# Kernel tuning notes

Hardware: AMD Instinct MI355X
Metric: run time of the kernel (lower is better)

Reference implementation:

```python
import jax, jax.numpy as jnp
import numpy as np


def setup_inputs() -> dict:
    key = jax.random.key(0)
    kx, ks = jax.random.split(key)
    M, N, D = 8192, 8192, 512
    X = jax.random.normal(kx, (M, D), dtype=jnp.float32)
    svs = jax.random.normal(ks, (N, D), dtype=jnp.float32)
    # scale = 1/(2*sigma^2); a plausible fitted value for standard-normal data
    scale = jnp.asarray(0.01, dtype=jnp.float32)
    return {"X": X, "svs": svs, "scale": scale}


def reference(X, svs, scale):
    N, D = svs.shape
    x2 = jnp.sum(X * X, axis=-1, keepdims=True)          # [M, 1]
    s2 = jnp.sum(svs * svs, axis=-1)                      # [N]
    dist2 = x2 + s2[None, :] - 2.0 * (X @ svs.T)          # [M, N]
    dist2 = jnp.maximum(dist2, 0.0)
    log_p = (jax.scipy.special.logsumexp(-scale * dist2, axis=-1)
             - jnp.log(jnp.asarray(N, dtype=X.dtype))
             + (D / 2) * jnp.log(scale / jnp.pi))
    return log_p
```

## Files before the change

### kernel.cpp

```cpp
#include <hip/hip_runtime.h>
#include <hip/hip_bf16.h>
#include <hip/hip_fp8.h>
#include <math.h>

typedef __attribute__((ext_vector_type(4))) int   int4v;
typedef __attribute__((ext_vector_type(8))) int   int8v;
typedef __attribute__((ext_vector_type(4))) float f32x4;

#define BM 128
#define BN 128
#define BK 128

__global__ __launch_bounds__(256) void prep_kernel(
    const float* __restrict__ X, const float* __restrict__ S,
    unsigned char* __restrict__ Xq, unsigned char* __restrict__ Sq,
    float* __restrict__ x2, float* __restrict__ s2,
    float* __restrict__ rowsum, int M, int R, int Dv)
{
    const int gid  = blockIdx.x * 256 + threadIdx.x;
    const int nthr = gridDim.x * 256;

    for (int i = gid; i < M; i += nthr) rowsum[i] = 0.f;

    const int lane = threadIdx.x & 63;
    const int wid  = gid >> 6;
    const int nw   = nthr >> 6;

    for (int row = wid; row < R; row += nw) {
        const float* rp;
        unsigned char* op;
        float* sq;
        if (row < M) { rp = X + (size_t)row * Dv;       op = Xq + (size_t)row * Dv;       sq = x2 + row; }
        else         { rp = S + (size_t)(row - M) * Dv; op = Sq + (size_t)(row - M) * Dv; sq = s2 + (row - M); }

        float acc = 0.f;
        for (int k = lane * 8; k < Dv; k += 64 * 8) {
            float4 v0 = *(const float4*)(rp + k);
            float4 v1 = *(const float4*)(rp + k + 4);
            acc += v0.x * v0.x + v0.y * v0.y + v0.z * v0.z + v0.w * v0.w;
            acc += v1.x * v1.x + v1.y * v1.y + v1.z * v1.z + v1.w * v1.w;
            union { __hip_fp8_e4m3 h[8]; uint2 u; } pk;
            pk.h[0] = __hip_fp8_e4m3(v0.x);
            pk.h[1] = __hip_fp8_e4m3(v0.y);
            pk.h[2] = __hip_fp8_e4m3(v0.z);
            pk.h[3] = __hip_fp8_e4m3(v0.w);
            pk.h[4] = __hip_fp8_e4m3(v1.x);
            pk.h[5] = __hip_fp8_e4m3(v1.y);
            pk.h[6] = __hip_fp8_e4m3(v1.z);
            pk.h[7] = __hip_fp8_e4m3(v1.w);
            *(uint2*)(op + k) = pk.u;
        }
#pragma unroll
        for (int off = 1; off < 64; off <<= 1)
            acc += __shfl_xor(acc, off, 64);
        if (lane == 0) *sq = acc;
    }
}

template<int DVC>
__global__ __launch_bounds__(256, 3) void kde_gemm_kernel(
    const unsigned char* __restrict__ Xq,
    const unsigned char* __restrict__ Sq,
    const float* __restrict__ x2,
    const float* __restrict__ s2,
    const float* __restrict__ scale_p,
    float* __restrict__ rowsum,
    int M, int N, int Dv)
{
    const int D = DVC ? DVC : Dv;

    __shared__ char smem[32768];
    unsigned char* As = (unsigned char*)smem;
    unsigned char* Bs = (unsigned char*)(smem + 16384);

    const int tid  = threadIdx.x;
    const int wave = tid >> 6;
    const int lane = tid & 63;
    const int quad = lane >> 4;
    const int l16  = lane & 15;

    const int m0 = blockIdx.x * BM;
    const int n0 = blockIdx.y * BN;
    const int wm = (wave & 1) * 64;
    const int wn = (wave >> 1) * 64;

    const float sc = *scale_p;

    f32x4 acc[4][4] = {};

    const int srow0 = wave * 8 + (lane >> 3);
    const int cg    = (lane & 7) ^ (lane >> 3);
    const unsigned char* gA = Xq + (size_t)(m0 + srow0) * D + cg * 16;
    const unsigned char* gB = Sq + (size_t)(n0 + srow0) * D + cg * 16;

#pragma unroll
    for (int k0 = 0; k0 < D; k0 += BK) {
        __syncthreads();
#pragma unroll
        for (int rd = 0; rd < 4; ++rd)
            __builtin_amdgcn_global_load_lds(
                (const __attribute__((address_space(1))) void*)(gA + (size_t)rd * 32 * D + k0),
                (__attribute__((address_space(3))) void*)(smem + rd * 4096 + wave * 1024),
                16, 0, 0);
#pragma unroll
        for (int rd = 0; rd < 4; ++rd)
            __builtin_amdgcn_global_load_lds(
                (const __attribute__((address_space(1))) void*)(gB + (size_t)rd * 32 * D + k0),
                (__attribute__((address_space(3))) void*)(smem + 16384 + rd * 4096 + wave * 1024),
                16, 0, 0);
        __syncthreads();

        const int e = l16 & 7;
        int8v a_frag[4], b_frag[4];
#pragma unroll
        for (int mi = 0; mi < 4; ++mi) {
            const unsigned char* rowp = As + (wm + mi * 16 + l16) * 128;
            int4v lo = *(const int4v*)(rowp + ((2 * quad)     ^ e) * 16);
            int4v hi = *(const int4v*)(rowp + ((2 * quad + 1) ^ e) * 16);
            a_frag[mi] = (int8v){lo.x, lo.y, lo.z, lo.w, hi.x, hi.y, hi.z, hi.w};
        }
#pragma unroll
        for (int ni = 0; ni < 4; ++ni) {
            const unsigned char* rowp = Bs + (wn + ni * 16 + l16) * 128;
            int4v lo = *(const int4v*)(rowp + ((2 * quad)     ^ e) * 16);
            int4v hi = *(const int4v*)(rowp + ((2 * quad + 1) ^ e) * 16);
            b_frag[ni] = (int8v){lo.x, lo.y, lo.z, lo.w, hi.x, hi.y, hi.z, hi.w};
        }
#pragma unroll
        for (int mi = 0; mi < 4; ++mi)
#pragma unroll
            for (int ni = 0; ni < 4; ++ni)
                acc[mi][ni] = __builtin_amdgcn_mfma_scale_f32_16x16x128_f8f6f4(
                    a_frag[mi], b_frag[ni], acc[mi][ni],
                    0, 0,
                    0, 0x7F7F7F7F,
                    0, 0x7F7F7F7F);
    }

    __syncthreads();
    float* wred = (float*)smem + wave * (64 * 20);

    float s2v[4];
#pragma unroll
    for (int ni = 0; ni < 4; ++ni)
        s2v[ni] = s2[n0 + wn + ni * 16 + l16];

#pragma unroll
    for (int mi = 0; mi < 4; ++mi) {
#pragma unroll
        for (int r = 0; r < 4; ++r) {
            const int rowL = mi * 16 + quad * 4 + r;
            const float xv = x2[m0 + wm + rowL];
            float sum = 0.f;
#pragma unroll
            for (int ni = 0; ni < 4; ++ni) {
                float d2 = xv + s2v[ni] - 2.0f * acc[mi][ni][r];
                d2 = fmaxf(d2, 0.f);
                sum += __expf(-sc * d2);
            }
            wred[rowL * 20 + l16] = sum;
        }
    }
    __syncthreads();

    float4 p0 = *(float4*)(wred + lane * 20 + 0);
    float4 p1 = *(float4*)(wred + lane * 20 + 4);
    float4 p2 = *(float4*)(wred + lane * 20 + 8);
    float4 p3 = *(float4*)(wred + lane * 20 + 12);
    float s = (p0.x + p0.y + p0.z + p0.w) + (p1.x + p1.y + p1.z + p1.w)
            + (p2.x + p2.y + p2.z + p2.w) + (p3.x + p3.y + p3.z + p3.w);
    atomicAdd(&rowsum[m0 + wm + lane], s);
}

__global__ void finalize_kernel(const float* __restrict__ rowsum,
                                const float* __restrict__ scale_p,
                                float* __restrict__ out, int M, int N, int Dv) {
    const int m = blockIdx.x * 256 + threadIdx.x;
    if (m < M) {
        const float sc = *scale_p;
        const float cst = -logf((float)N) + 0.5f * (float)Dv * logf(sc / 3.14159265358979f);
        out[m] = logf(rowsum[m]) + cst;
    }
}

extern "C" void kernel_launch(void* const* d_in, const int* in_sizes, int n_in,
                              void* d_out, int out_size, void* d_ws, size_t ws_size,
                              hipStream_t stream) {
    const float* X       = (const float*)d_in[0];
    const float* S       = (const float*)d_in[1];
    const float* scale_p = (const float*)d_in[2];
    float* out = (float*)d_out;

    const int M  = out_size;
    const int Dv = in_sizes[0] / M;
    const int N  = in_sizes[1] / Dv;

    char* ws = (char*)d_ws;
    unsigned char* Xq = (unsigned char*)ws;
    unsigned char* Sq = (unsigned char*)(ws + (size_t)M * Dv);
    float* x2     = (float*)(ws + (size_t)M * Dv + (size_t)N * Dv);
    float* s2     = x2 + M;
    float* rowsum = s2 + N;

    prep_kernel<<<512, 256, 0, stream>>>(X, S, Xq, Sq, x2, s2, rowsum, M, M + N, Dv);

    dim3 grid(M / BM, N / BN);
    if (Dv == 512)
        kde_gemm_kernel<512><<<grid, 256, 0, stream>>>(Xq, Sq, x2, s2, scale_p, rowsum, M, N, Dv);
    else
        kde_gemm_kernel<0><<<grid, 256, 0, stream>>>(Xq, Sq, x2, s2, scale_p, rowsum, M, N, Dv);

    finalize_kernel<<<(M + 255) / 256, 256, 0, stream>>>(rowsum, scale_p, out, M, N, Dv);
}
```

Baseline: 122.1 us.

## Specialize D=512 GEMM: full-K B tile in LDS, A fragments in registers

Adds a dedicated kernel for D=512. It loads the whole 128x512 fp8 block of support vectors into 64KB of LDS in a single pass and reads each wave's 32 A rows straight from global memory into registers. This removes the per-K-step syncs and staging of A. Each wave now covers 32 rows by all 128 columns, so every B fragment loaded from LDS feeds two MFMAs. The costs are double the LDS, occupancy dropping from 3 to 2 blocks, no overlap of loads with compute, and uncoalesced register loads for A.

```diff
diff --git a/kernel.cpp b/kernel.cpp
--- a/kernel.cpp
+++ b/kernel.cpp
@@ -7,9 +7,8 @@
 typedef __attribute__((ext_vector_type(8))) int   int8v;
 typedef __attribute__((ext_vector_type(4))) float f32x4;
 
-#define BM 128
-#define BN 128
-#define BK 128
+#define AS1 __attribute__((address_space(1)))
+#define AS3 __attribute__((address_space(3)))
 
 __global__ __launch_bounds__(256) void prep_kernel(
     const float* __restrict__ X, const float* __restrict__ S,
@@ -57,21 +56,17 @@
     }
 }
 
-template<int DVC>
-__global__ __launch_bounds__(256, 3) void kde_gemm_kernel(
+__global__ __launch_bounds__(256, 2) void kde_gemm512(
     const unsigned char* __restrict__ Xq,
     const unsigned char* __restrict__ Sq,
     const float* __restrict__ x2,
     const float* __restrict__ s2,
     const float* __restrict__ scale_p,
     float* __restrict__ rowsum,
-    int M, int N, int Dv)
+    int M, int N)
 {
-    const int D = DVC ? DVC : Dv;
-
-    __shared__ char smem[32768];
-    unsigned char* As = (unsigned char*)smem;
-    unsigned char* Bs = (unsigned char*)(smem + 16384);
+    __shared__ char smem[65536];
+    unsigned char* Bs = (unsigned char*)smem;
 
     const int tid  = threadIdx.x;
     const int wave = tid >> 6;
@@ -79,13 +74,113 @@
     const int quad = lane >> 4;
     const int l16  = lane & 15;
 
-    const int m0 = blockIdx.x * BM;
-    const int n0 = blockIdx.y * BN;
+    const int m0 = blockIdx.x * 128;
+    const int n0 = blockIdx.y * 128;
+
+    const float sc = *scale_p;
+
+    const int srow = tid >> 5;
+    const int cg   = (tid & 31) ^ srow;
+    const unsigned char* gB = Sq + (size_t)(n0 + srow) * 512 + cg * 16;
+#pragma unroll
+    for (int r = 0; r < 16; ++r)
+        __builtin_amdgcn_global_load_lds(
+            (const AS1 void*)(gB + (size_t)r * 8 * 512),
+            (AS3 void*)(smem + r * 4096 + wave * 1024),
+            16, 0, 0);
+
+    int8v af[2][4];
+    const unsigned char* gA = Xq + (size_t)(m0 + wave * 32 + l16) * 512 + quad * 32;
+#pragma unroll
+    for (int mi = 0; mi < 2; ++mi)
+#pragma unroll
+        for (int c = 0; c < 4; ++c) {
+            int4v lo = *(const int4v*)(gA + mi * 16 * 512 + c * 128);
+            int4v hi = *(const int4v*)(gA + mi * 16 * 512 + c * 128 + 16);
+            af[mi][c] = (int8v){lo.x, lo.y, lo.z, lo.w, hi.x, hi.y, hi.z, hi.w};
+        }
+
+    f32x4 acc[2][8] = {};
+
+    __syncthreads();
+
+    const int e = l16 & 7;
+#pragma unroll
+    for (int c = 0; c < 4; ++c) {
+#pragma unroll
+        for (int ni = 0; ni < 8; ++ni) {
+            const unsigned char* rowp = Bs + (size_t)(ni * 16 + l16) * 512;
+            int4v lo = *(const int4v*)(rowp + (8 * c + ((2 * quad)     ^ e)) * 16);
+            int4v hi = *(const int4v*)(rowp + (8 * c + ((2 * quad + 1) ^ e)) * 16);
+            int8v bf = (int8v){lo.x, lo.y, lo.z, lo.w, hi.x, hi.y, hi.z, hi.w};
+            acc[0][ni] = __builtin_amdgcn_mfma_scale_f32_16x16x128_f8f6f4(
+                af[0][c], bf, acc[0][ni], 0, 0, 0, 0x7F7F7F7F, 0, 0x7F7F7F7F);
+            acc[1][ni] = __builtin_amdgcn_mfma_scale_f32_16x16x128_f8f6f4(
+                af[1][c], bf, acc[1][ni], 0, 0, 0, 0x7F7F7F7F, 0, 0x7F7F7F7F);
+        }
+    }
+
+    __syncthreads();
+    float* wred = (float*)smem + wave * (32 * 20);
+
+    float s2v[8];
+#pragma unroll
+    for (int ni = 0; ni < 8; ++ni)
+        s2v[ni] = s2[n0 + ni * 16 + l16];
+
+#pragma unroll
+    for (int mi = 0; mi < 2; ++mi) {
+#pragma unroll
+        for (int r = 0; r < 4; ++r) {
+            const int rl = mi * 16 + quad * 4 + r;
+            const float xv = x2[m0 + wave * 32 + rl];
+            float sum = 0.f;
+#pragma unroll
+            for (int ni = 0; ni < 8; ++ni) {
+                float d2 = xv + s2v[ni] - 2.0f * acc[mi][ni][r];
+                d2 = fmaxf(d2, 0.f);
+                sum += __expf(-sc * d2);
+            }
+            wred[rl * 20 + l16] = sum;
+        }
+    }
+    __syncthreads();
+
+    if (lane < 32) {
+        float* rp = wred + lane * 20;
+        float4 p0 = *(float4*)(rp + 0);
+        float4 p1 = *(float4*)(rp + 4);
+        float4 p2 = *(float4*)(rp + 8);
+        float4 p3 = *(float4*)(rp + 12);
+        float s = (p0.x + p0.y + p0.z + p0.w) + (p1.x + p1.y + p1.z + p1.w)
+                + (p2.x + p2.y + p2.z + p2.w) + (p3.x + p3.y + p3.z + p3.w);
+        atomicAdd(&rowsum[m0 + wave * 32 + lane], s);
+    }
+}
+
+__global__ __launch_bounds__(256, 3) void kde_gemm_generic(
+    const unsigned char* __restrict__ Xq, const unsigned char* __restrict__ Sq,
+    const float* __restrict__ x2, const float* __restrict__ s2,
+    const float* __restrict__ scale_p, float* __restrict__ rowsum,
+    int M, int N, int Dv)
+{
+    const int D = Dv;
+    __shared__ char smem[32768];
+    unsigned char* As = (unsigned char*)smem;
+    unsigned char* Bs = (unsigned char*)(smem + 16384);
+
+    const int tid  = threadIdx.x;
+    const int wave = tid >> 6;
+    const int lane = tid & 63;
+    const int quad = lane >> 4;
+    const int l16  = lane & 15;
+
+    const int m0 = blockIdx.x * 128;
+    const int n0 = blockIdx.y * 128;
     const int wm = (wave & 1) * 64;
     const int wn = (wave >> 1) * 64;
 
     const float sc = *scale_p;
-
     f32x4 acc[4][4] = {};
 
     const int srow0 = wave * 8 + (lane >> 3);
@@ -93,21 +188,18 @@
     const unsigned char* gA = Xq + (size_t)(m0 + srow0) * D + cg * 16;
     const unsigned char* gB = Sq + (size_t)(n0 + srow0) * D + cg * 16;
 
-#pragma unroll
-    for (int k0 = 0; k0 < D; k0 += BK) {
+    for (int k0 = 0; k0 < D; k0 += 128) {
         __syncthreads();
 #pragma unroll
         for (int rd = 0; rd < 4; ++rd)
             __builtin_amdgcn_global_load_lds(
-                (const __attribute__((address_space(1))) void*)(gA + (size_t)rd * 32 * D + k0),
-                (__attribute__((address_space(3))) void*)(smem + rd * 4096 + wave * 1024),
-                16, 0, 0);
+                (const AS1 void*)(gA + (size_t)rd * 32 * D + k0),
+                (AS3 void*)(smem + rd * 4096 + wave * 1024), 16, 0, 0);
 #pragma unroll
         for (int rd = 0; rd < 4; ++rd)
             __builtin_amdgcn_global_load_lds(
-                (const __attribute__((address_space(1))) void*)(gB + (size_t)rd * 32 * D + k0),
-                (__attribute__((address_space(3))) void*)(smem + 16384 + rd * 4096 + wave * 1024),
-                16, 0, 0);
+                (const AS1 void*)(gB + (size_t)rd * 32 * D + k0),
+                (AS3 void*)(smem + 16384 + rd * 4096 + wave * 1024), 16, 0, 0);
         __syncthreads();
 
         const int e = l16 & 7;
@@ -132,9 +224,7 @@
             for (int ni = 0; ni < 4; ++ni)
                 acc[mi][ni] = __builtin_amdgcn_mfma_scale_f32_16x16x128_f8f6f4(
                     a_frag[mi], b_frag[ni], acc[mi][ni],
-                    0, 0,
-                    0, 0x7F7F7F7F,
-                    0, 0x7F7F7F7F);
+                    0, 0, 0, 0x7F7F7F7F, 0, 0x7F7F7F7F);
     }
 
     __syncthreads();
@@ -204,11 +294,11 @@
 
     prep_kernel<<<512, 256, 0, stream>>>(X, S, Xq, Sq, x2, s2, rowsum, M, M + N, Dv);
 
-    dim3 grid(M / BM, N / BN);
+    dim3 grid(M / 128, N / 128);
     if (Dv == 512)
-        kde_gemm_kernel<512><<<grid, 256, 0, stream>>>(Xq, Sq, x2, s2, scale_p, rowsum, M, N, Dv);
+        kde_gemm512<<<grid, 256, 0, stream>>>(Xq, Sq, x2, s2, scale_p, rowsum, M, N);
     else
-        kde_gemm_kernel<0><<<grid, 256, 0, stream>>>(Xq, Sq, x2, s2, scale_p, rowsum, M, N, Dv);
+        kde_gemm_generic<<<grid, 256, 0, stream>>>(Xq, Sq, x2, s2, scale_p, rowsum, M, N, Dv);
 
     finalize_kernel<<<(M + 255) / 256, 256, 0, stream>>>(rowsum, scale_p, out, M, N, Dv);
 }
```

Result: slower. 141.7 us (+16.0%).
